# Optimization experiments

Measured on AMD Instinct MI355X. Metric: run time of the kernel, lower is better.

## Reference

```python
import jax, jax.numpy as jnp
from jax import lax
import numpy as np

EPS = 1e-5  # torch BatchNorm2d default eps


def _conv(x, w, b):
    # NCHW conv, stride 1, 'same' padding (matches nn.Conv2d(padding='same'))
    y = lax.conv_general_dilated(x, w, (1, 1), 'SAME',
                                 dimension_numbers=('NCHW', 'OIHW', 'NCHW'))
    return y + b[None, :, None, None]


def _bn(x, g, b, m, v):
    # eval-mode BatchNorm2d using running stats
    s = g * lax.rsqrt(v + EPS)
    return x * s[None, :, None, None] + (b - m * s)[None, :, None, None]


def _pool(x):
    # MaxPool2d(2, 2)
    return lax.reduce_window(x, -jnp.inf, lax.max, (1, 1, 2, 2), (1, 1, 2, 2), 'VALID')


def setup_inputs() -> dict:
    key = jax.random.key(0)
    ks = list(jax.random.split(key, 16))
    B, H, W = 64, 128, 128
    chans = [1, 32, 64, 96]
    R, C_LRLC, HL, WL = 4, 128, 16, 16
    FC1, NCLS = 512, 10

    def nrm(k, shape, fan_in):
        return jax.random.normal(k, shape, jnp.float32) / np.float32(np.sqrt(fan_in))

    inp = {"x": jax.random.normal(ks[0], (B, 1, H, W), jnp.float32)}
    for i in range(3):
        ci, co = chans[i], chans[i + 1]
        inp[f"conv{i+1}_w"] = nrm(ks[1 + i], (co, ci, 3, 3), ci * 9)
        inp[f"conv{i+1}_b"] = jnp.zeros((co,), jnp.float32)
        inp[f"bn{i+1}_g"] = jnp.ones((co,), jnp.float32)
        inp[f"bn{i+1}_b"] = jnp.zeros((co,), jnp.float32)
        inp[f"bn{i+1}_m"] = 0.1 * jax.random.normal(ks[4 + i], (co,), jnp.float32)
        inp[f"bn{i+1}_v"] = jax.random.uniform(ks[7 + i], (co,), jnp.float32, 0.5, 1.5)
    # LRLC basis filters: R basis kernels stacked along out-channel dim
    inp["basis_w"] = nrm(ks[10], (R * C_LRLC, chans[-1], 3, 3), chans[-1] * 9)
    inp["basis_b"] = jnp.zeros((R, C_LRLC), jnp.float32)  # per-rank bias basis
    # OuterCombiningWeights: row/col logits, softmax over rank per location
    inp["cw_h"] = 0.1 * jax.random.normal(ks[11], (HL, R), jnp.float32)
    inp["cw_w"] = 0.1 * jax.random.normal(ks[12], (WL, R), jnp.float32)
    inp["fc1_w"] = nrm(ks[13], (FC1, HL * WL * C_LRLC), HL * WL * C_LRLC)
    inp["fc1_b"] = jnp.zeros((FC1,), jnp.float32)
    inp["fc2_w"] = nrm(ks[14], (NCLS, FC1), FC1)
    inp["fc2_b"] = jnp.zeros((NCLS,), jnp.float32)
    return inp


def reference(x, conv1_w, conv1_b, bn1_g, bn1_b, bn1_m, bn1_v,
              conv2_w, conv2_b, bn2_g, bn2_b, bn2_m, bn2_v,
              conv3_w, conv3_b, bn3_g, bn3_b, bn3_m, bn3_v,
              basis_w, basis_b, cw_h, cw_w, fc1_w, fc1_b, fc2_w, fc2_b):
    blocks = ((conv1_w, conv1_b, bn1_g, bn1_b, bn1_m, bn1_v),
              (conv2_w, conv2_b, bn2_g, bn2_b, bn2_m, bn2_v),
              (conv3_w, conv3_b, bn3_g, bn3_b, bn3_m, bn3_v))
    for cw_, cb_, g_, b_, m_, v_ in blocks:  # conv -> BN -> ReLU -> pool
        x = _pool(jax.nn.relu(_bn(_conv(x, cw_, cb_), g_, b_, m_, v_)))

    R, C = basis_b.shape
    # combining weights: softmax over rank at each (h, w)
    cw = jax.nn.softmax(cw_h[:, None, :] + cw_w[None, :, :], axis=-1)  # (HL, WL, R)
    # R basis convolutions in one call, then per-location low-rank combine
    y = lax.conv_general_dilated(x, basis_w, (1, 1), 'SAME',
                                 dimension_numbers=('NCHW', 'OIHW', 'NCHW'))
    B, _, HL, WL = y.shape
    y = y.reshape(B, R, C, HL, WL)
    out = jnp.einsum('brchw,hwr->bchw', y, cw)
    out = out + jnp.einsum('hwr,rc->chw', cw, basis_b)[None]  # low-rank spatial bias
    out = jax.nn.relu(out)
    out = out.reshape(B, -1)
    out = jax.nn.relu(out @ fc1_w.T + fc1_b)
    return out @ fc2_w.T + fc2_b
```

## Files before the change

### kernel.cpp

```cpp
#include <hip/hip_runtime.h>
#include <hip/hip_bf16.h>

#define EPS 1e-5f

typedef short s16x8 __attribute__((ext_vector_type(8)));
typedef float f32x4 __attribute__((ext_vector_type(4)));

__device__ __forceinline__ unsigned short f2bf(float f) {
    unsigned u = __float_as_uint(f);
    u += 0x7fffu + ((u >> 16) & 1u);
    return (unsigned short)(u >> 16);
}

__global__ __launch_bounds__(256) void repack_w(
    const float* __restrict__ c2w, const float* __restrict__ c3w,
    const float* __restrict__ bw,
    const float* __restrict__ c1w, const float* __restrict__ c1b,
    const float* __restrict__ b1g, const float* __restrict__ b1b,
    const float* __restrict__ b1m, const float* __restrict__ b1v,
    unsigned short* __restrict__ wp2S, unsigned short* __restrict__ wp3F,
    unsigned short* __restrict__ wpL3, float* __restrict__ wf1)
{
    int idx = blockIdx.x * 256 + threadIdx.x;
    if (idx < 18432) {
        int ch = idx >> 3, e = idx & 7;
        int co = ch / 36, rem = ch % 36;
        int s = rem >> 2, slot = rem & 3;
        int g = slot ^ ((co >> 1) & 3);
        int ci = g * 8 + e;
        wp2S[idx] = f2bf(c2w[(co * 32 + ci) * 9 + s]);
    } else if (idx < 73728) {
        int i = idx - 18432;
        int e    = i & 7;
        int lane = (i >> 3) & 63;
        int f    = i >> 9;
        int cg   = f % 6;
        int t2   = f / 6;
        int kk   = t2 & 1;
        int s    = t2 >> 1;
        int col = lane & 15, quad = lane >> 4;
        int co = cg * 16 + col;
        int ci = (kk * 4 + quad) * 8 + e;
        wp3F[i] = f2bf(c3w[(co * 64 + ci) * 9 + s]);
    } else if (idx < 516096) {
        int i = idx - 73728;
        int e    = i & 7;
        int lane = (i >> 3) & 63;
        int fk   = i >> 9;
        int kk   = fk % 3;
        int t    = fk / 3;
        int j    = t & 1;
        int rp   = (t >> 1) & 1;
        int g    = (t >> 2) & 1;
        int cbk  = (t >> 3) & 3;
        int s    = t >> 5;
        int col = lane & 15, quad = lane >> 4;
        int cog = (rp * 2 + j) * 128 + cbk * 32 + g * 16 + col;
        int ci  = (kk * 4 + quad) * 8 + e;
        wpL3[i] = f2bf(bw[(cog * 96 + ci) * 9 + s]);
    } else if (idx < 516416) {
        int i = idx - 516096;
        int co = i / 10, k = i % 10;
        float scl = b1g[co] * rsqrtf(b1v[co] + EPS);
        wf1[i] = (k < 9) ? c1w[co * 9 + k] * scl
                         : (c1b[co] - b1m[co]) * scl + b1b[co];
    }
}

__global__ __launch_bounds__(256) void conv1_h(
    const float* __restrict__ x,
    const float* __restrict__ wf1,
    unsigned short* __restrict__ out)
{
    __shared__ float xs[4][132];

    const int tid = threadIdx.x;
    const int b = blockIdx.x >> 6, ph = blockIdx.x & 63;

    for (int i = tid; i < 4 * 132; i += 256) ((float*)xs)[i] = 0.f;
    __syncthreads();
    const int row0 = 2 * ph - 1;
    for (int i = tid; i < 4 * 128; i += 256) {
        int r = i >> 7, c = i & 127;
        int gr = row0 + r;
        if (gr >= 0 && gr < 128)
            xs[r][c + 1] = x[(size_t)b * 16384 + gr * 128 + c];
    }
    __syncthreads();

    const int pw = tid & 63, wavei = tid >> 6;
    float pr[4][4];
    #pragma unroll
    for (int rr = 0; rr < 4; ++rr) {
        float2 u0 = *(const float2*)&xs[rr][2 * pw];
        float2 u1 = *(const float2*)&xs[rr][2 * pw + 2];
        pr[rr][0] = u0.x; pr[rr][1] = u0.y; pr[rr][2] = u1.x; pr[rr][3] = u1.y;
    }

    const float* wb = wf1 + wavei * 80;
    s16x8 res;
    #pragma unroll
    for (int c8 = 0; c8 < 8; ++c8) {
        const float* wv = wb + c8 * 10;
        float a00 = 0.f, a01 = 0.f, a10 = 0.f, a11 = 0.f;
        #pragma unroll
        for (int ky = 0; ky < 3; ++ky)
            #pragma unroll
            for (int kx = 0; kx < 3; ++kx) {
                float wk = wv[ky * 3 + kx];
                a00 = fmaf(wk, pr[ky][kx],         a00);
                a01 = fmaf(wk, pr[ky][kx + 1],     a01);
                a10 = fmaf(wk, pr[ky + 1][kx],     a10);
                a11 = fmaf(wk, pr[ky + 1][kx + 1], a11);
            }
        float o = fmaxf(fmaxf(fmaxf(a00, a01), fmaxf(a10, a11)) + wv[9], 0.f);
        res[c8] = (short)f2bf(o);
    }
    *(s16x8*)(out + (((size_t)(b * 64 + ph)) * 64 + pw) * 32 + wavei * 8) = res;
}

__global__ __launch_bounds__(256) void conv2_mfma(
    const unsigned short* __restrict__ xin,
    const unsigned short* __restrict__ wp2S,
    const float* __restrict__ cbv, const float* __restrict__ gg,
    const float* __restrict__ bnb, const float* __restrict__ mm,
    const float* __restrict__ vv,
    unsigned short* __restrict__ out)
{
    constexpr int CI = 32, CO = 64, W = 64, WT = 66, CG = 4;
    constexpr int ASZ = 4 * WT * CI * 2;
    constexpr int BSZ = 9 * CO * CI * 2;
    constexpr int PH2 = 32, HPX = 4;

    __shared__ __align__(16) unsigned char sm[ASZ + BSZ];

    const int tid = threadIdx.x;
    const int wave = tid >> 6, lane = tid & 63;
    const int quad = lane >> 4, col = lane & 15;
    const int wm = wave;

    const int xcd  = blockIdx.x & 7;
    const int slot = blockIdx.x >> 3;
    const int hp = xcd * HPX + (slot % HPX);
    const int b  = slot / HPX;

    constexpr int NCHA = 4 * WT * CG;
    for (int ch = tid; ch < NCHA; ch += 256) {
        int r    = ch / (WT * CG);
        int rem  = ch % (WT * CG);
        int wp   = rem / CG;
        int slot_ = rem % CG;
        int g = slot_ ^ ((wp >> 1) & 3);
        int h = hp * 2 - 1 + r;
        int w = wp - 1;
        s16x8 val = {};
        if (h >= 0 && h < W && w >= 0 && w < W)
            val = *(const s16x8*)(xin + (((size_t)(b * W + h) * W + w) * CI + g * 8));
        *(s16x8*)(sm + ch * 16) = val;
    }
    for (int ch = tid; ch < 2304; ch += 256)
        *(s16x8*)(sm + ASZ + ch * 16) = *(const s16x8*)(wp2S + ch * 8);
    __syncthreads();

    f32x4 acc[2][4];
    #pragma unroll
    for (int i = 0; i < 2; ++i)
        #pragma unroll
        for (int j = 0; j < 4; ++j) acc[i][j] = (f32x4){0.f, 0.f, 0.f, 0.f};

    #pragma unroll
    for (int s = 0; s < 9; ++s) {
        const int dy = s / 3, dx = s % 3;
        const int g = quad;
        s16x8 a[2];
        #pragma unroll
        for (int mi = 0; mi < 2; ++mi) {
            int wp = wm * 16 + col + dx;
            int r  = mi + dy;
            int addr = (r * WT + wp) * (CI * 2) + ((g ^ ((wp >> 1) & 3)) << 4);
            a[mi] = *(const s16x8*)(sm + addr);
        }
        #pragma unroll
        for (int nf = 0; nf < 4; ++nf) {
            int co_l = nf * 16 + col;
            int row = co_l * 9 + s;
            int addr = ASZ + row * (CI * 2) + ((g ^ ((co_l >> 1) & 3)) << 4);
            s16x8 bf = *(const s16x8*)(sm + addr);
            acc[0][nf] = __builtin_amdgcn_mfma_f32_16x16x32_bf16(a[0], bf, acc[0][nf], 0, 0, 0);
            acc[1][nf] = __builtin_amdgcn_mfma_f32_16x16x32_bf16(a[1], bf, acc[1][nf], 0, 0, 0);
        }
    }

    #pragma unroll
    for (int nf = 0; nf < 4; ++nf) {
        int co = nf * 16 + col;
        float scl = gg[co] * rsqrtf(vv[co] + EPS);
        float sh  = (cbv[co] - mm[co]) * scl + bnb[co];
        #pragma unroll
        for (int pr = 0; pr < 2; ++pr) {
            float y0 = fmaf(acc[0][nf][2 * pr],     scl, sh);
            float y1 = fmaf(acc[0][nf][2 * pr + 1], scl, sh);
            float y2 = fmaf(acc[1][nf][2 * pr],     scl, sh);
            float y3 = fmaf(acc[1][nf][2 * pr + 1], scl, sh);
            float o = fmaxf(fmaxf(fmaxf(y0, y1), fmaxf(y2, y3)), 0.f);
            int pw = wm * 8 + quad * 2 + pr;
            out[((size_t)(b * PH2 + hp) * PH2 + pw) * CO + co] = f2bf(o);
        }
    }
}

__global__ __launch_bounds__(256) void conv3_mfma(
    const unsigned short* __restrict__ xin,
    const unsigned short* __restrict__ wp3F,
    const float* __restrict__ cbv, const float* __restrict__ gg,
    const float* __restrict__ bnb, const float* __restrict__ mm,
    const float* __restrict__ vv,
    unsigned short* __restrict__ out)
{
    constexpr int CI = 64, CO = 96, W = 32, WT = 34, CG = 8;
    constexpr int ASZ = 4 * WT * CI * 2;
    constexpr int PH2 = 16, HPX = 2;

    __shared__ __align__(16) unsigned char sm[ASZ];

    const int tid = threadIdx.x;
    const int wave = tid >> 6, lane = tid & 63;
    const int quad = lane >> 4, col = lane & 15;
    const int wm = wave & 1, wn = wave >> 1;

    const int xcd  = blockIdx.x & 7;
    const int slot = blockIdx.x >> 3;
    const int hp = xcd * HPX + (slot % HPX);
    const int b  = slot / HPX;

    constexpr int NCHA = 4 * WT * CG;
    for (int ch = tid; ch < NCHA; ch += 256) {
        int r    = ch / (WT * CG);
        int rem  = ch % (WT * CG);
        int wp   = rem / CG;
        int slot_ = rem % CG;
        int g = slot_ ^ (wp & 7);
        int h = hp * 2 - 1 + r;
        int w = wp - 1;
        s16x8 val = {};
        if (h >= 0 && h < W && w >= 0 && w < W)
            val = *(const s16x8*)(xin + (((size_t)(b * W + h) * W + w) * CI + g * 8));
        *(s16x8*)(sm + ch * 16) = val;
    }
    __syncthreads();

    f32x4 acc[2][3];
    #pragma unroll
    for (int i = 0; i < 2; ++i)
        #pragma unroll
        for (int j = 0; j < 3; ++j) acc[i][j] = (f32x4){0.f, 0.f, 0.f, 0.f};

    for (int s = 0; s < 9; ++s) {
        const int dy = s / 3, dx = s % 3;
        s16x8 bf[3][2];
        #pragma unroll
        for (int nf = 0; nf < 3; ++nf)
            #pragma unroll
            for (int kk = 0; kk < 2; ++kk) {
                int fidx = (((s * 2 + kk) * 6) + wn * 3 + nf) * 512 + lane * 8;
                bf[nf][kk] = *(const s16x8*)(wp3F + fidx);
            }
        #pragma unroll
        for (int kk = 0; kk < 2; ++kk) {
            const int g = kk * 4 + quad;
            s16x8 a[2];
            #pragma unroll
            for (int mi = 0; mi < 2; ++mi) {
                int wp = wm * 16 + col + dx;
                int r  = mi + dy;
                int addr = (r * WT + wp) * (CI * 2) + ((g ^ (wp & 7)) << 4);
                a[mi] = *(const s16x8*)(sm + addr);
            }
            #pragma unroll
            for (int nf = 0; nf < 3; ++nf) {
                acc[0][nf] = __builtin_amdgcn_mfma_f32_16x16x32_bf16(a[0], bf[nf][kk], acc[0][nf], 0, 0, 0);
                acc[1][nf] = __builtin_amdgcn_mfma_f32_16x16x32_bf16(a[1], bf[nf][kk], acc[1][nf], 0, 0, 0);
            }
        }
    }

    #pragma unroll
    for (int nf = 0; nf < 3; ++nf) {
        int co = (wn * 3 + nf) * 16 + col;
        float scl = gg[co] * rsqrtf(vv[co] + EPS);
        float sh  = (cbv[co] - mm[co]) * scl + bnb[co];
        #pragma unroll
        for (int pr = 0; pr < 2; ++pr) {
            float y0 = fmaf(acc[0][nf][2 * pr],     scl, sh);
            float y1 = fmaf(acc[0][nf][2 * pr + 1], scl, sh);
            float y2 = fmaf(acc[1][nf][2 * pr],     scl, sh);
            float y3 = fmaf(acc[1][nf][2 * pr + 1], scl, sh);
            float o = fmaxf(fmaxf(fmaxf(y0, y1), fmaxf(y2, y3)), 0.f);
            int pw = wm * 8 + quad * 2 + pr;
            out[((size_t)(b * PH2 + hp) * PH2 + pw) * CO + co] = f2bf(o);
        }
    }
}

__global__ __launch_bounds__(512) void lrlc_mfma4(
    const unsigned short* __restrict__ xin,
    const unsigned short* __restrict__ wpk3,
    const float* __restrict__ bbias,
    const float* __restrict__ cwh, const float* __restrict__ cww,
    unsigned short* __restrict__ actB)
{
    constexpr int CI = 96, WT = 18, NR = 10, CG = 12;
    constexpr int ASZ = NR * WT * CI * 2;
    __shared__ __align__(16) unsigned char sm[ASZ];
    __shared__ float cwt[256][4];

    const int tid = threadIdx.x;
    const int wave = tid >> 6, lane = tid & 63;
    const int quad = lane >> 4, col = lane & 15;
    const int wm = wave & 1;
    const int g  = (wave >> 1) & 1;
    const int rp = wave >> 2;

    const int cbk = blockIdx.x & 3;
    const int mb  = (blockIdx.x >> 2) & 1;
    const int b   = blockIdx.x >> 3;

    if (tid < 256) {
        int h = tid >> 4, w = tid & 15;
        float e[4], mx = -1e30f;
        #pragma unroll
        for (int r = 0; r < 4; ++r) { e[r] = cwh[h * 4 + r] + cww[w * 4 + r]; mx = fmaxf(mx, e[r]); }
        float se = 0.f;
        #pragma unroll
        for (int r = 0; r < 4; ++r) { e[r] = expf(e[r] - mx); se += e[r]; }
        float inv = 1.f / se;
        #pragma unroll
        for (int r = 0; r < 4; ++r) cwt[tid][r] = e[r] * inv;
    }

    constexpr int NCHA = NR * WT * CG;
    for (int ch = tid; ch < NCHA; ch += 512) {
        int r    = ch / (WT * CG);
        int rem  = ch % (WT * CG);
        int wp   = rem / CG, slot = rem % CG;
        int gg_ = slot ^ ((wp >> 1) & 3);
        int h = mb * 8 + r - 1;
        int w = wp - 1;
        s16x8 val = {};
        if (h >= 0 && h < 16 && w >= 0 && w < 16)
            val = *(const s16x8*)(xin + (((size_t)(b * 16 + h) * 16 + w) * CI + gg_ * 8));
        *(s16x8*)(sm + ch * 16) = val;
    }
    __syncthreads();

    f32x4 acc[4][2];
    #pragma unroll
    for (int i = 0; i < 4; ++i)
        #pragma unroll
        for (int j = 0; j < 2; ++j) acc[i][j] = (f32x4){0.f, 0.f, 0.f, 0.f};

    const int tbase = ((cbk * 2 + g) * 2 + rp);
    for (int s = 0; s < 9; ++s) {
        const int dy = s / 3, dx = s % 3;
        s16x8 bf[2][3];
        #pragma unroll
        for (int j = 0; j < 2; ++j)
            #pragma unroll
            for (int kk = 0; kk < 3; ++kk) {
                int fidx = ((s * 32 + tbase * 2 + j) * 3 + kk) * 512 + lane * 8;
                bf[j][kk] = *(const s16x8*)(wpk3 + fidx);
            }
        #pragma unroll
        for (int kk = 0; kk < 3; ++kk) {
            const int gg = kk * 4 + quad;
            s16x8 a[4];
            #pragma unroll
            for (int mi = 0; mi < 4; ++mi) {
                int mf = wm * 4 + mi;
                int r  = mf + dy;
                int wp = col + dx;
                int addr = (r * WT + wp) * (CI * 2) + ((gg ^ ((wp >> 1) & 3)) << 4);
                a[mi] = *(const s16x8*)(sm + addr);
            }
            #pragma unroll
            for (int mi = 0; mi < 4; ++mi)
                #pragma unroll
                for (int j = 0; j < 2; ++j)
                    acc[mi][j] = __builtin_amdgcn_mfma_f32_16x16x32_bf16(
                        a[mi], bf[j][kk], acc[mi][j], 0, 0, 0);
        }
    }
    __syncthreads();

    float* ldo = (float*)sm;
    {
        const int c_lo = g * 16 + col;
        const int cg   = cbk * 32 + c_lo;
        float bbA = bbias[(rp * 2 + 0) * 128 + cg];
        float bbB = bbias[(rp * 2 + 1) * 128 + cg];
        #pragma unroll
        for (int mi = 0; mi < 4; ++mi) {
            int mf = wm * 4 + mi;
            #pragma unroll
            for (int rg = 0; rg < 4; ++rg) {
                int hwl = mf * 16 + quad * 4 + rg;
                int hwg = mb * 128 + hwl;
                float o = cwt[hwg][rp * 2]     * (acc[mi][0][rg] + bbA)
                        + cwt[hwg][rp * 2 + 1] * (acc[mi][1][rg] + bbB);
                ldo[(rp * 128 + hwl) * 33 + c_lo] = o;
            }
        }
    }
    __syncthreads();
    {
        int cl = tid >> 4;
        int sg = tid & 15;
        size_t base = (size_t)b * 32768 + (cbk * 32 + cl) * 256 + mb * 128 + sg * 8;
        s16x8 v;
        #pragma unroll
        for (int i = 0; i < 8; ++i) {
            int hw = sg * 8 + i;
            float o = ldo[hw * 33 + cl] + ldo[(128 + hw) * 33 + cl];
            v[i] = (short)f2bf(fmaxf(o, 0.f));
        }
        *(s16x8*)(actB + base) = v;
    }
}

__global__ __launch_bounds__(256) void fc1_lds(
    const unsigned short* __restrict__ actB,
    const float* __restrict__ w,
    float* __restrict__ partial)
{
    __shared__ __align__(16) unsigned short Wl[64 * 256];
    __shared__ __align__(16) unsigned short Al[64 * 256];

    const int tid = threadIdx.x;
    const int wave = tid >> 6, lane = tid & 63;
    const int quad = lane >> 4, col = lane & 15;
    const int wm = wave & 1, wn = wave >> 1;
    const int xcd  = blockIdx.x & 7;
    const int slot = blockIdx.x >> 3;
    const int ks = xcd * 8 + (slot >> 3);
    const int jt = slot & 7;

    const int rt  = tid >> 2;
    const int seg = tid & 3;

    const float* wsrc = w + (size_t)(jt * 64 + rt) * 32768 + ks * 512 + seg * 64;
    const unsigned short* asrc = actB + (size_t)rt * 32768 + ks * 512 + seg * 64;

    f32x4 acc[2][2];
    #pragma unroll
    for (int i = 0; i < 2; ++i)
        #pragma unroll
        for (int j = 0; j < 2; ++j) acc[i][j] = (f32x4){0.f, 0.f, 0.f, 0.f};

    float4 pw0[8], pw1[8]; s16x8 pa[8];
    #pragma unroll
    for (int u = 0; u < 8; ++u) {
        pw0[u] = *(const float4*)(wsrc + u * 8);
        pw1[u] = *(const float4*)(wsrc + u * 8 + 4);
        pa[u]  = *(const s16x8*)(asrc + u * 8);
    }

    #pragma unroll
    for (int c = 0; c < 2; ++c) {
        #pragma unroll
        for (int u = 0; u < 8; ++u) {
            s16x8 v;
            v[0] = (short)f2bf(pw0[u].x); v[1] = (short)f2bf(pw0[u].y);
            v[2] = (short)f2bf(pw0[u].z); v[3] = (short)f2bf(pw0[u].w);
            v[4] = (short)f2bf(pw1[u].x); v[5] = (short)f2bf(pw1[u].y);
            v[6] = (short)f2bf(pw1[u].z); v[7] = (short)f2bf(pw1[u].w);
            int phys = (seg * 8 + u) ^ (rt & 7);
            *(s16x8*)(Wl + rt * 256 + phys * 8) = v;
            *(s16x8*)(Al + rt * 256 + phys * 8) = pa[u];
        }
        __syncthreads();
        if (c == 0) {
            #pragma unroll
            for (int u = 0; u < 8; ++u) {
                pw0[u] = *(const float4*)(wsrc + 256 + u * 8);
                pw1[u] = *(const float4*)(wsrc + 256 + u * 8 + 4);
                pa[u]  = *(const s16x8*)(asrc + 256 + u * 8);
            }
        }
        #pragma unroll
        for (int kk = 0; kk < 8; ++kk) {
            const int gg = kk * 4 + quad;
            s16x8 a[2], bb[2];
            #pragma unroll
            for (int mf = 0; mf < 2; ++mf) {
                int j_l = wm * 32 + mf * 16 + col;
                a[mf] = *(const s16x8*)(Wl + j_l * 256 + ((gg ^ (j_l & 7)) << 3));
            }
            #pragma unroll
            for (int bg = 0; bg < 2; ++bg) {
                int b_l = wn * 32 + bg * 16 + col;
                bb[bg] = *(const s16x8*)(Al + b_l * 256 + ((gg ^ (b_l & 7)) << 3));
            }
            #pragma unroll
            for (int mf = 0; mf < 2; ++mf)
                #pragma unroll
                for (int bg = 0; bg < 2; ++bg)
                    acc[mf][bg] = __builtin_amdgcn_mfma_f32_16x16x32_bf16(
                        a[mf], bb[bg], acc[mf][bg], 0, 0, 0);
        }
        __syncthreads();
    }
    #pragma unroll
    for (int mf = 0; mf < 2; ++mf)
        #pragma unroll
        for (int bg = 0; bg < 2; ++bg)
            #pragma unroll
            for (int r = 0; r < 4; ++r) {
                int j = jt * 64 + wm * 32 + mf * 16 + quad * 4 + r;
                int b = wn * 32 + bg * 16 + col;
                partial[((size_t)ks * 512 + j) * 64 + b] = acc[mf][bg][r];
            }
}

__global__ __launch_bounds__(256) void fc1_reduce4(
    const float* __restrict__ partial, const float* __restrict__ bias,
    float* __restrict__ out)
{
    int idx = blockIdx.x * 256 + threadIdx.x;
    int b = idx & 63, j = idx >> 6;
    float a = bias[j];
    #pragma unroll 8
    for (int ks = 0; ks < 64; ++ks)
        a += partial[((size_t)ks * 512 + j) * 64 + b];
    out[b * 512 + j] = fmaxf(a, 0.f);
}

__global__ __launch_bounds__(320) void fc2_w(
    const float* __restrict__ xin,
    const float* __restrict__ w,
    const float* __restrict__ bias,
    float* __restrict__ out)
{
    const int b = blockIdx.x;
    const int tid = threadIdx.x;
    const int n = tid >> 5, l = tid & 31;
    const float* xr = xin + b * 512 + l * 16;
    const float* wr = w + n * 512 + l * 16;
    float s = 0.f;
    #pragma unroll
    for (int u = 0; u < 4; ++u) {
        float4 xv = *(const float4*)(xr + u * 4);
        float4 wv = *(const float4*)(wr + u * 4);
        s = fmaf(xv.x, wv.x, s); s = fmaf(xv.y, wv.y, s);
        s = fmaf(xv.z, wv.z, s); s = fmaf(xv.w, wv.w, s);
    }
    #pragma unroll
    for (int off = 16; off > 0; off >>= 1)
        s += __shfl_xor(s, off, 32);
    if (l == 0) out[b * 10 + n] = s + bias[n];
}

extern "C" void kernel_launch(void* const* d_in, const int* in_sizes, int n_in,
                              void* d_out, int out_size, void* d_ws, size_t ws_size,
                              hipStream_t stream) {
    const float* x   = (const float*)d_in[0];
    const float* c1w = (const float*)d_in[1];  const float* c1b = (const float*)d_in[2];
    const float* b1g = (const float*)d_in[3];  const float* b1b = (const float*)d_in[4];
    const float* b1m = (const float*)d_in[5];  const float* b1v = (const float*)d_in[6];
    const float* c2w = (const float*)d_in[7];  const float* c2b = (const float*)d_in[8];
    const float* b2g = (const float*)d_in[9];  const float* b2b = (const float*)d_in[10];
    const float* b2m = (const float*)d_in[11]; const float* b2v = (const float*)d_in[12];
    const float* c3w = (const float*)d_in[13]; const float* c3b = (const float*)d_in[14];
    const float* b3g = (const float*)d_in[15]; const float* b3b = (const float*)d_in[16];
    const float* b3m = (const float*)d_in[17]; const float* b3v = (const float*)d_in[18];
    const float* bw  = (const float*)d_in[19]; const float* bb  = (const float*)d_in[20];
    const float* cwh = (const float*)d_in[21]; const float* cww = (const float*)d_in[22];
    const float* f1w = (const float*)d_in[23]; const float* f1b = (const float*)d_in[24];
    const float* f2w = (const float*)d_in[25]; const float* f2b = (const float*)d_in[26];
    float* out = (float*)d_out;

    char* ws = (char*)d_ws;
    unsigned short* act1 = (unsigned short*)(ws + 0);
    unsigned short* act2 = (unsigned short*)(ws + 16777216);
    unsigned short* act3 = (unsigned short*)(ws + 0);
    unsigned short* actB = (unsigned short*)(ws + 4194304);
    float*          part = (float*)(ws + 8388608);
    float*          fc1o = (float*)(ws + 0);
    unsigned short* wp2S = (unsigned short*)(ws + 25165824);
    unsigned short* wp3F = (unsigned short*)(ws + 25202688);
    unsigned short* wpL3 = (unsigned short*)(ws + 25313280);
    float*          wf1  = (float*)(ws + 26198016);

    repack_w<<<2018, 256, 0, stream>>>(c2w, c3w, bw, c1w, c1b, b1g, b1b, b1m, b1v,
                                       wp2S, wp3F, wpL3, wf1);

    conv1_h<<<4096, 256, 0, stream>>>(x, wf1, act1);

    conv2_mfma<<<2048, 256, 0, stream>>>(act1, wp2S, c2b, b2g, b2b, b2m, b2v, act2);

    conv3_mfma<<<1024, 256, 0, stream>>>(act2, wp3F, c3b, b3g, b3b, b3m, b3v, act3);

    lrlc_mfma4<<<512, 512, 0, stream>>>(act3, wpL3, bb, cwh, cww, actB);

    fc1_lds<<<512, 256, 0, stream>>>(actB, f1w, part);
    fc1_reduce4<<<128, 256, 0, stream>>>(part, f1b, fc1o);
    fc2_w<<<64, 320, 0, stream>>>(fc1o, f2w, f2b, out);
}
```

Measured before the change: 101.1 us.

## Fuse weight repack into conv1 launch and split fc1 K across more blocks

Merges the weight repack kernel and conv1 into one launch: the first 4096 blocks run conv1, computing the folded BN conv1 weights in shared memory, and the remaining blocks repack the conv2, conv3 and LRLC weights. This removes one kernel launch and the wf1 round trip through global memory. fc1 now uses 1024 blocks, each covering a 256-wide K slice in a single LDS load-then-compute phase, replacing the two-stage register prefetch. The reduce kernel sums 128 partials instead of 64. The trade is more partial-sum traffic and extra per-block BN folding work in exchange for more parallelism and fewer launches.

```diff
diff --git a/kernel.cpp b/kernel.cpp
--- a/kernel.cpp
+++ b/kernel.cpp
@@ -12,72 +12,73 @@
     return (unsigned short)(u >> 16);
 }
 
-__global__ __launch_bounds__(256) void repack_w(
-    const float* __restrict__ c2w, const float* __restrict__ c3w,
-    const float* __restrict__ bw,
+__global__ __launch_bounds__(256) void repack_conv1(
+    const float* __restrict__ x,
     const float* __restrict__ c1w, const float* __restrict__ c1b,
     const float* __restrict__ b1g, const float* __restrict__ b1b,
     const float* __restrict__ b1m, const float* __restrict__ b1v,
+    const float* __restrict__ c2w, const float* __restrict__ c3w,
+    const float* __restrict__ bw,
+    unsigned short* __restrict__ act1,
     unsigned short* __restrict__ wp2S, unsigned short* __restrict__ wp3F,
-    unsigned short* __restrict__ wpL3, float* __restrict__ wf1)
-{
-    int idx = blockIdx.x * 256 + threadIdx.x;
-    if (idx < 18432) {
-        int ch = idx >> 3, e = idx & 7;
-        int co = ch / 36, rem = ch % 36;
-        int s = rem >> 2, slot = rem & 3;
-        int g = slot ^ ((co >> 1) & 3);
-        int ci = g * 8 + e;
-        wp2S[idx] = f2bf(c2w[(co * 32 + ci) * 9 + s]);
-    } else if (idx < 73728) {
-        int i = idx - 18432;
-        int e    = i & 7;
-        int lane = (i >> 3) & 63;
-        int f    = i >> 9;
-        int cg   = f % 6;
-        int t2   = f / 6;
-        int kk   = t2 & 1;
-        int s    = t2 >> 1;
-        int col = lane & 15, quad = lane >> 4;
-        int co = cg * 16 + col;
-        int ci = (kk * 4 + quad) * 8 + e;
-        wp3F[i] = f2bf(c3w[(co * 64 + ci) * 9 + s]);
-    } else if (idx < 516096) {
-        int i = idx - 73728;
-        int e    = i & 7;
-        int lane = (i >> 3) & 63;
-        int fk   = i >> 9;
-        int kk   = fk % 3;
-        int t    = fk / 3;
-        int j    = t & 1;
-        int rp   = (t >> 1) & 1;
-        int g    = (t >> 2) & 1;
-        int cbk  = (t >> 3) & 3;
-        int s    = t >> 5;
-        int col = lane & 15, quad = lane >> 4;
-        int cog = (rp * 2 + j) * 128 + cbk * 32 + g * 16 + col;
-        int ci  = (kk * 4 + quad) * 8 + e;
-        wpL3[i] = f2bf(bw[(cog * 96 + ci) * 9 + s]);
-    } else if (idx < 516416) {
-        int i = idx - 516096;
+    unsigned short* __restrict__ wpL3)
+{
+    const int tid = threadIdx.x;
+    if (blockIdx.x >= 4096) {
+        int idx = (blockIdx.x - 4096) * 256 + tid;
+        if (idx < 18432) {
+            int ch = idx >> 3, e = idx & 7;
+            int co = ch / 36, rem = ch % 36;
+            int s = rem >> 2, slot = rem & 3;
+            int g = slot ^ ((co >> 1) & 3);
+            int ci = g * 8 + e;
+            wp2S[idx] = f2bf(c2w[(co * 32 + ci) * 9 + s]);
+        } else if (idx < 73728) {
+            int i = idx - 18432;
+            int e    = i & 7;
+            int lane = (i >> 3) & 63;
+            int f    = i >> 9;
+            int cg   = f % 6;
+            int t2   = f / 6;
+            int kk   = t2 & 1;
+            int s    = t2 >> 1;
+            int col = lane & 15, quad = lane >> 4;
+            int co = cg * 16 + col;
+            int ci = (kk * 4 + quad) * 8 + e;
+            wp3F[i] = f2bf(c3w[(co * 64 + ci) * 9 + s]);
+        } else if (idx < 516096) {
+            int i = idx - 73728;
+            int e    = i & 7;
+            int lane = (i >> 3) & 63;
+            int fk   = i >> 9;
+            int kk   = fk % 3;
+            int t    = fk / 3;
+            int j    = t & 1;
+            int rp   = (t >> 1) & 1;
+            int g    = (t >> 2) & 1;
+            int cbk  = (t >> 3) & 3;
+            int s    = t >> 5;
+            int col = lane & 15, quad = lane >> 4;
+            int cog = (rp * 2 + j) * 128 + cbk * 32 + g * 16 + col;
+            int ci  = (kk * 4 + quad) * 8 + e;
+            wpL3[i] = f2bf(bw[(cog * 96 + ci) * 9 + s]);
+        }
+        return;
+    }
+
+    __shared__ float xs[4][132];
+    __shared__ float wfs[320];
+
+    const int bid = blockIdx.x;
+    const int b = bid >> 6, ph = bid & 63;
+
+    for (int i = tid; i < 4 * 132; i += 256) ((float*)xs)[i] = 0.f;
+    for (int i = tid; i < 320; i += 256) {
         int co = i / 10, k = i % 10;
         float scl = b1g[co] * rsqrtf(b1v[co] + EPS);
-        wf1[i] = (k < 9) ? c1w[co * 9 + k] * scl
+        wfs[i] = (k < 9) ? c1w[co * 9 + k] * scl
                          : (c1b[co] - b1m[co]) * scl + b1b[co];
     }
-}
-
-__global__ __launch_bounds__(256) void conv1_h(
-    const float* __restrict__ x,
-    const float* __restrict__ wf1,
-    unsigned short* __restrict__ out)
-{
-    __shared__ float xs[4][132];
-
-    const int tid = threadIdx.x;
-    const int b = blockIdx.x >> 6, ph = blockIdx.x & 63;
-
-    for (int i = tid; i < 4 * 132; i += 256) ((float*)xs)[i] = 0.f;
     __syncthreads();
     const int row0 = 2 * ph - 1;
     for (int i = tid; i < 4 * 128; i += 256) {
@@ -97,7 +98,7 @@
         pr[rr][0] = u0.x; pr[rr][1] = u0.y; pr[rr][2] = u1.x; pr[rr][3] = u1.y;
     }
 
-    const float* wb = wf1 + wavei * 80;
+    const float* wb = wfs + wavei * 80;
     s16x8 res;
     #pragma unroll
     for (int c8 = 0; c8 < 8; ++c8) {
@@ -116,7 +117,7 @@
         float o = fmaxf(fmaxf(fmaxf(a00, a01), fmaxf(a10, a11)) + wv[9], 0.f);
         res[c8] = (short)f2bf(o);
     }
-    *(s16x8*)(out + (((size_t)(b * 64 + ph)) * 64 + pw) * 32 + wavei * 8) = res;
+    *(s16x8*)(act1 + (((size_t)(b * 64 + ph)) * 64 + pw) * 32 + wavei * 8) = res;
 }
 
 __global__ __launch_bounds__(256) void conv2_mfma(
@@ -427,7 +428,7 @@
     }
 }
 
-__global__ __launch_bounds__(256) void fc1_lds(
+__global__ __launch_bounds__(256) void fc1_stream(
     const unsigned short* __restrict__ actB,
     const float* __restrict__ w,
     float* __restrict__ partial)
@@ -441,14 +442,31 @@
     const int wm = wave & 1, wn = wave >> 1;
     const int xcd  = blockIdx.x & 7;
     const int slot = blockIdx.x >> 3;
-    const int ks = xcd * 8 + (slot >> 3);
+    const int ks = xcd * 16 + (slot >> 3);
     const int jt = slot & 7;
+    const int k0 = ks * 256;
 
     const int rt  = tid >> 2;
     const int seg = tid & 3;
 
-    const float* wsrc = w + (size_t)(jt * 64 + rt) * 32768 + ks * 512 + seg * 64;
-    const unsigned short* asrc = actB + (size_t)rt * 32768 + ks * 512 + seg * 64;
+    const float* wsrc = w + (size_t)(jt * 64 + rt) * 32768 + k0 + seg * 64;
+    const unsigned short* asrc = actB + (size_t)rt * 32768 + k0 + seg * 64;
+
+    #pragma unroll
+    for (int u = 0; u < 8; ++u) {
+        float4 f0 = *(const float4*)(wsrc + u * 8);
+        float4 f1 = *(const float4*)(wsrc + u * 8 + 4);
+        s16x8 av = *(const s16x8*)(asrc + u * 8);
+        s16x8 v;
+        v[0] = (short)f2bf(f0.x); v[1] = (short)f2bf(f0.y);
+        v[2] = (short)f2bf(f0.z); v[3] = (short)f2bf(f0.w);
+        v[4] = (short)f2bf(f1.x); v[5] = (short)f2bf(f1.y);
+        v[6] = (short)f2bf(f1.z); v[7] = (short)f2bf(f1.w);
+        int phys = (seg * 8 + u) ^ (rt & 7);
+        *(s16x8*)(Wl + rt * 256 + phys * 8) = v;
+        *(s16x8*)(Al + rt * 256 + phys * 8) = av;
+    }
+    __syncthreads();
 
     f32x4 acc[2][2];
     #pragma unroll
@@ -456,58 +474,26 @@
         #pragma unroll
         for (int j = 0; j < 2; ++j) acc[i][j] = (f32x4){0.f, 0.f, 0.f, 0.f};
 
-    float4 pw0[8], pw1[8]; s16x8 pa[8];
-    #pragma unroll
-    for (int u = 0; u < 8; ++u) {
-        pw0[u] = *(const float4*)(wsrc + u * 8);
-        pw1[u] = *(const float4*)(wsrc + u * 8 + 4);
-        pa[u]  = *(const s16x8*)(asrc + u * 8);
-    }
-
-    #pragma unroll
-    for (int c = 0; c < 2; ++c) {
-        #pragma unroll
-        for (int u = 0; u < 8; ++u) {
-            s16x8 v;
-            v[0] = (short)f2bf(pw0[u].x); v[1] = (short)f2bf(pw0[u].y);
-            v[2] = (short)f2bf(pw0[u].z); v[3] = (short)f2bf(pw0[u].w);
-            v[4] = (short)f2bf(pw1[u].x); v[5] = (short)f2bf(pw1[u].y);
-            v[6] = (short)f2bf(pw1[u].z); v[7] = (short)f2bf(pw1[u].w);
-            int phys = (seg * 8 + u) ^ (rt & 7);
-            *(s16x8*)(Wl + rt * 256 + phys * 8) = v;
-            *(s16x8*)(Al + rt * 256 + phys * 8) = pa[u];
-        }
-        __syncthreads();
-        if (c == 0) {
-            #pragma unroll
-            for (int u = 0; u < 8; ++u) {
-                pw0[u] = *(const float4*)(wsrc + 256 + u * 8);
-                pw1[u] = *(const float4*)(wsrc + 256 + u * 8 + 4);
-                pa[u]  = *(const s16x8*)(asrc + 256 + u * 8);
-            }
-        }
-        #pragma unroll
-        for (int kk = 0; kk < 8; ++kk) {
-            const int gg = kk * 4 + quad;
-            s16x8 a[2], bb[2];
-            #pragma unroll
-            for (int mf = 0; mf < 2; ++mf) {
-                int j_l = wm * 32 + mf * 16 + col;
-                a[mf] = *(const s16x8*)(Wl + j_l * 256 + ((gg ^ (j_l & 7)) << 3));
-            }
-            #pragma unroll
-            for (int bg = 0; bg < 2; ++bg) {
-                int b_l = wn * 32 + bg * 16 + col;
-                bb[bg] = *(const s16x8*)(Al + b_l * 256 + ((gg ^ (b_l & 7)) << 3));
-            }
-            #pragma unroll
-            for (int mf = 0; mf < 2; ++mf)
-                #pragma unroll
-                for (int bg = 0; bg < 2; ++bg)
-                    acc[mf][bg] = __builtin_amdgcn_mfma_f32_16x16x32_bf16(
-                        a[mf], bb[bg], acc[mf][bg], 0, 0, 0);
-        }
-        __syncthreads();
+    #pragma unroll
+    for (int kk = 0; kk < 8; ++kk) {
+        const int gg = kk * 4 + quad;
+        s16x8 a[2], bb[2];
+        #pragma unroll
+        for (int mf = 0; mf < 2; ++mf) {
+            int j_l = wm * 32 + mf * 16 + col;
+            a[mf] = *(const s16x8*)(Wl + j_l * 256 + ((gg ^ (j_l & 7)) << 3));
+        }
+        #pragma unroll
+        for (int bg = 0; bg < 2; ++bg) {
+            int b_l = wn * 32 + bg * 16 + col;
+            bb[bg] = *(const s16x8*)(Al + b_l * 256 + ((gg ^ (b_l & 7)) << 3));
+        }
+        #pragma unroll
+        for (int mf = 0; mf < 2; ++mf)
+            #pragma unroll
+            for (int bg = 0; bg < 2; ++bg)
+                acc[mf][bg] = __builtin_amdgcn_mfma_f32_16x16x32_bf16(
+                    a[mf], bb[bg], acc[mf][bg], 0, 0, 0);
     }
     #pragma unroll
     for (int mf = 0; mf < 2; ++mf)
@@ -521,15 +507,15 @@
             }
 }
 
-__global__ __launch_bounds__(256) void fc1_reduce4(
+__global__ __launch_bounds__(256) void fc1_reduce6(
     const float* __restrict__ partial, const float* __restrict__ bias,
     float* __restrict__ out)
 {
     int idx = blockIdx.x * 256 + threadIdx.x;
     int b = idx & 63, j = idx >> 6;
     float a = bias[j];
-    #pragma unroll 8
-    for (int ks = 0; ks < 64; ++ks)
+    #pragma unroll 16
+    for (int ks = 0; ks < 128; ++ks)
         a += partial[((size_t)ks * 512 + j) * 64 + b];
     out[b * 512 + j] = fmaxf(a, 0.f);
 }
@@ -588,12 +574,9 @@
     unsigned short* wp2S = (unsigned short*)(ws + 25165824);
     unsigned short* wp3F = (unsigned short*)(ws + 25202688);
     unsigned short* wpL3 = (unsigned short*)(ws + 25313280);
-    float*          wf1  = (float*)(ws + 26198016);
-
-    repack_w<<<2018, 256, 0, stream>>>(c2w, c3w, bw, c1w, c1b, b1g, b1b, b1m, b1v,
-                                       wp2S, wp3F, wpL3, wf1);
-
-    conv1_h<<<4096, 256, 0, stream>>>(x, wf1, act1);
+
+    repack_conv1<<<6112, 256, 0, stream>>>(x, c1w, c1b, b1g, b1b, b1m, b1v,
+                                           c2w, c3w, bw, act1, wp2S, wp3F, wpL3);
 
     conv2_mfma<<<2048, 256, 0, stream>>>(act1, wp2S, c2b, b2g, b2b, b2m, b2v, act2);
 
@@ -601,7 +584,7 @@
 
     lrlc_mfma4<<<512, 512, 0, stream>>>(act3, wpL3, bb, cwh, cww, actB);
 
-    fc1_lds<<<512, 256, 0, stream>>>(actB, f1w, part);
-    fc1_reduce4<<<128, 256, 0, stream>>>(part, f1b, fc1o);
+    fc1_stream<<<1024, 256, 0, stream>>>(actB, f1w, part);
+    fc1_reduce6<<<128, 256, 0, stream>>>(part, f1b, fc1o);
     fc2_w<<<64, 320, 0, stream>>>(fc1o, f2w, f2b, out);
 }
```

Result: faster. 97.63 us (median of 2 runs) (-3.4%).
